# Kernel optimization log

Measured on AMD Instinct MI355X. Metric: run time of the kernel, lower is better.

## Reference

```python
import jax
import jax.numpy as jnp
from jax import lax
import numpy as np

INPUT_DIM = 784
HIDDEN_DIM = 1024
BATCH = 256
N_BINS = 10


def setup_inputs() -> dict:
    key = jax.random.key(0)
    k1, k2, k3, k4, k5 = jax.random.split(key, 5)
    # kaiming-normal-ish init scales (faithful in spirit; exact values irrelevant for math)
    W = jax.random.normal(k1, (HIDDEN_DIM, INPUT_DIM), dtype=jnp.float32) * np.sqrt(2.0 / INPUT_DIM)
    c = jnp.zeros((HIDDEN_DIM, 1), dtype=jnp.float32)
    V = jax.random.normal(k2, (INPUT_DIM, HIDDEN_DIM, N_BINS), dtype=jnp.float32) * np.sqrt(2.0 / N_BINS)
    b = jnp.zeros((INPUT_DIM, N_BINS), dtype=jnp.float32)
    x = jax.random.randint(k3, (BATCH, INPUT_DIM), 0, N_BINS, dtype=jnp.int32)
    return {"x": x, "W": W, "c": c, "V": V, "b": b}


def reference(x, W, c, V, b):
    # x: [B, D] int pixel bins; W: [H, D]; c: [H, 1]; V: [D, H, 10]; b: [D, 10]
    B = x.shape[0]
    xf = x.astype(jnp.float32)  # [B, D]
    a0 = jnp.broadcast_to(c[:, 0][None, :], (B, W.shape[0]))  # [B, H]

    def step(a, inp):
        Vi, bi, Wi, xi = inp  # Vi:[H,10], bi:[10], Wi:[H], xi:[B]
        h = jax.nn.sigmoid(a)                       # [B, H]
        p = jax.nn.softmax(h @ Vi + bi, axis=1)     # [B, 10]
        a = a + xi[:, None] * Wi[None, :]           # rank-1 update, matches x_i @ W[:,i].T
        return a, p

    _, p_seq = lax.scan(step, a0, (V, b, W.T, xf.T))  # p_seq: [D, B, 10]
    p_hat = jnp.transpose(p_seq, (1, 2, 0))            # [B, 10, D] == torch.stack(p_hat, dim=2)
    return p_hat
```

## Files before the change

kernel.cpp:

```cpp
#include <hip/hip_runtime.h>
#include <stdint.h>

#define D_DIM 784
#define H_DIM 1024
#define B_DIM 256
#define NBIN  10
#define G_CH  8
#define T_CH  98
#define BT    16
#define BF    4
#define LOG2E 1.4426950408889634f

typedef _Float16 half8_t  __attribute__((ext_vector_type(8)));
typedef __fp16   fp16x2_t __attribute__((ext_vector_type(2)));
typedef float    float4_t __attribute__((ext_vector_type(4)));

__global__ void k_transpose(const float* __restrict__ W, float* __restrict__ Wt2) {
    __shared__ float t[64][65];
    int j0 = blockIdx.x * 64, h0 = blockIdx.y * 64;
    int tj = threadIdx.x & 63, tr = threadIdx.x >> 6;
    int j = j0 + tj;
    #pragma unroll
    for (int r = 0; r < 16; ++r) {
        int hh = tr * 16 + r;
        t[hh][tj] = (j < D_DIM) ? W[(size_t)(h0 + hh) * D_DIM + j] : 0.0f;
    }
    __syncthreads();
    #pragma unroll
    for (int r = 0; r < 16; ++r) {
        int jj = tr * 16 + r;
        int jo = j0 + jj;
        if (jo < D_DIM) Wt2[(size_t)jo * H_DIM + h0 + tj] = t[tj][jj] * LOG2E;
    }
}

__global__ void k_vbprep(const float* __restrict__ V, _Float16* __restrict__ VB) {
    int i   = blockIdx.x;
    int tid = threadIdx.x;
    __shared__ __align__(16) float vsf[H_DIM * NBIN];
    const float4* src = (const float4*)(V + (size_t)i * H_DIM * NBIN);
    #pragma unroll
    for (int q = 0; q < 10; ++q) {
        float4 v = src[q * 256 + tid];
        *((float4*)&vsf[(q * 256 + tid) * 4]) = v;
    }
    __syncthreads();
    #pragma unroll
    for (int q = 0; q < 8; ++q) {
        int pair = q * 256 + tid;
        int kk = pair >> 6, l = pair & 63;
        int n = l & 15, hb = kk * 32 + ((l >> 4) & 3) * 8;
        union { _Float16 h[8]; uint4 u; } o;
        #pragma unroll
        for (int jj = 0; jj < 8; ++jj)
            o.h[jj] = (_Float16)((n < NBIN) ? vsf[(hb + jj) * NBIN + n] : 0.0f);
        ((uint4*)VB)[(size_t)i * 2048 + pair] = o.u;
    }
}

template<typename CT>
__global__ void k_pscan(const float* __restrict__ Wt2, const int* __restrict__ x,
                        const float* __restrict__ c, CT* __restrict__ PA) {
    int b0 = blockIdx.x * BF;
    int h  = blockIdx.y * 256 + threadIdx.x;
    __shared__ float xs[BF][D_DIM];
    for (int q = threadIdx.x; q < BF * (D_DIM / 4); q += 256) {
        int bb = q / (D_DIM / 4), r = q % (D_DIM / 4);
        int4 xi = ((const int4*)(x + (size_t)(b0 + bb) * D_DIM))[r];
        float4 xf = make_float4((float)xi.x, (float)xi.y, (float)xi.z, (float)xi.w);
        *((float4*)&xs[bb][r * 4]) = xf;
    }
    float acc[BF];
    float cv = c[h] * LOG2E;
    #pragma unroll
    for (int bb = 0; bb < BF; ++bb) acc[bb] = cv;
    __syncthreads();
    for (int t = 0; t < T_CH; ++t) {
        #pragma unroll
        for (int bb = 0; bb < BF; ++bb)
            PA[((size_t)t * B_DIM + b0 + bb) * H_DIM + h] = (CT)acc[bb];
        #pragma unroll
        for (int j = 0; j < G_CH; ++j) {
            float wv = Wt2[(size_t)(t * G_CH + j) * H_DIM + h];
            #pragma unroll
            for (int bb = 0; bb < BF; ++bb)
                acc[bb] += xs[bb][t * G_CH + j] * wv;
        }
    }
}

template<typename CT>
__global__ __launch_bounds__(256, 2)
void k_main(const float* __restrict__ Wt2, const _Float16* __restrict__ VB,
            const CT* __restrict__ PA, const int* __restrict__ x,
            const float* __restrict__ bias, float* __restrict__ out) {
    int bt  = blockIdx.x;
    int tc  = blockIdx.y;
    int tid = threadIdx.x;
    int w   = tid >> 6;
    int l   = tid & 63;
    int bl  = l & 15;
    int kg  = l >> 4;
    int bg  = bt * BT + bl;
    int i0  = tc * G_CH;

    __shared__ __align__(16) float wlds[G_CH][H_DIM];
    __shared__ float red[2][4][64][5];
    __shared__ float bs[G_CH][16];
    __shared__ __align__(16) float plds[BT][NBIN][12];

    {
        int ii = tid >> 4, n = tid & 15;
        if (ii < G_CH) bs[ii][n] = (n < NBIN) ? bias[(size_t)(i0 + ii) * NBIN + n] : 0.0f;
    }
    {
        #pragma unroll
        for (int r = 0; r < G_CH; ++r) {
            float4 v = ((const float4*)(Wt2 + (size_t)(i0 + r) * H_DIM))[tid];
            *((float4*)&wlds[r][tid * 4]) = v;
        }
    }
    float xvf[G_CH];
    {
        const int4* xp = (const int4*)(x + (size_t)bg * D_DIM + i0);
        int4 x0 = xp[0], x1 = xp[1];
        xvf[0] = (float)x0.x; xvf[1] = (float)x0.y; xvf[2] = (float)x0.z; xvf[3] = (float)x0.w;
        xvf[4] = (float)x1.x; xvf[5] = (float)x1.y; xvf[6] = (float)x1.z; xvf[7] = (float)x1.w;
    }
    float a[8][8];
    {
        const CT* src = PA + ((size_t)tc * B_DIM + bg) * H_DIM + w * 256 + kg * 8;
        #pragma unroll
        for (int m = 0; m < 8; ++m)
            #pragma unroll
            for (int j = 0; j < 8; ++j)
                a[m][j] = (float)src[m * 32 + j];
    }
    __syncthreads();

    const uint4* vbbase = (const uint4*)VB;
    #pragma unroll 1
    for (int ii = 0; ii < G_CH; ++ii) {
        int i = i0 + ii;
        int par = ii & 1;

        uint4 vb[8];
        const uint4* vbp = vbbase + ((size_t)i * 32 + w * 8) * 64 + l;
        #pragma unroll
        for (int m = 0; m < 8; ++m) vb[m] = vbp[m * 64];

        if (ii > 0) {
            int ip = ii - 1, pp = par ^ 1;
            float tot = red[pp][0][l][w] + red[pp][1][l][w] + red[pp][2][l][w] + red[pp][3][l][w];
            int n = bl;
            float v = (n < NBIN) ? tot + bs[ip][n] : -3.0e38f;
            float vm = v;
            vm = fmaxf(vm, __shfl_xor(vm, 1));
            vm = fmaxf(vm, __shfl_xor(vm, 2));
            vm = fmaxf(vm, __shfl_xor(vm, 4));
            vm = fmaxf(vm, __shfl_xor(vm, 8));
            float e = __builtin_amdgcn_exp2f((v - vm) * LOG2E);
            float ss = e;
            ss += __shfl_xor(ss, 1); ss += __shfl_xor(ss, 2);
            ss += __shfl_xor(ss, 4); ss += __shfl_xor(ss, 8);
            float p = e * __builtin_amdgcn_rcpf(ss);
            if (n < NBIN) plds[kg * 4 + w][n][ip] = p;
        }

        float xf = xvf[ii];
        float4_t cfrag = {0.f, 0.f, 0.f, 0.f};
        #pragma unroll
        for (int m = 0; m < 8; ++m) {
            union { half8_t h8; uint u32[4]; } af;
            #pragma unroll
            for (int p = 0; p < 4; ++p) {
                float s0 = __builtin_amdgcn_rcpf(1.0f + __builtin_amdgcn_exp2f(-a[m][2 * p]));
                float s1 = __builtin_amdgcn_rcpf(1.0f + __builtin_amdgcn_exp2f(-a[m][2 * p + 1]));
                union { fp16x2_t v; uint u; } cv;
                cv.v = __builtin_amdgcn_cvt_pkrtz(s0, s1);
                af.u32[p] = cv.u;
            }
            union { half8_t h8; uint4 u; } bf;
            bf.u = vb[m];
            cfrag = __builtin_amdgcn_mfma_f32_16x16x32_f16(af.h8, bf.h8, cfrag, 0, 0, 0);

            const float4* wrow = (const float4*)&wlds[ii][w * 256 + kg * 8];
            float4 w0 = wrow[m * 8];
            float4 w1 = wrow[m * 8 + 1];
            a[m][0] += xf * w0.x; a[m][1] += xf * w0.y; a[m][2] += xf * w0.z; a[m][3] += xf * w0.w;
            a[m][4] += xf * w1.x; a[m][5] += xf * w1.y; a[m][6] += xf * w1.z; a[m][7] += xf * w1.w;
        }

        red[par][w][l][0] = cfrag[0]; red[par][w][l][1] = cfrag[1];
        red[par][w][l][2] = cfrag[2]; red[par][w][l][3] = cfrag[3];
        __syncthreads();
    }
    {
        int ip = G_CH - 1, pp = (G_CH - 1) & 1;
        float tot = red[pp][0][l][w] + red[pp][1][l][w] + red[pp][2][l][w] + red[pp][3][l][w];
        int n = bl;
        float v = (n < NBIN) ? tot + bs[ip][n] : -3.0e38f;
        float vm = v;
        vm = fmaxf(vm, __shfl_xor(vm, 1));
        vm = fmaxf(vm, __shfl_xor(vm, 2));
        vm = fmaxf(vm, __shfl_xor(vm, 4));
        vm = fmaxf(vm, __shfl_xor(vm, 8));
        float e = __builtin_amdgcn_exp2f((v - vm) * LOG2E);
        float ss = e;
        ss += __shfl_xor(ss, 1); ss += __shfl_xor(ss, 2);
        ss += __shfl_xor(ss, 4); ss += __shfl_xor(ss, 8);
        float p = e * __builtin_amdgcn_rcpf(ss);
        if (n < NBIN) plds[kg * 4 + w][n][ip] = p;
    }
    __syncthreads();

    if (tid < BT * NBIN) {
        int bb = tid / NBIN, n = tid % NBIN;
        size_t base = ((size_t)(bt * BT + bb) * NBIN + n) * D_DIM + i0;
        #pragma unroll
        for (int q = 0; q < 2; ++q) {
            float4 v = *((float4*)&plds[bb][n][q * 4]);
            *((float4*)(out + base + q * 4)) = v;
        }
    }
}

extern "C" void kernel_launch(void* const* d_in, const int* in_sizes, int n_in,
                              void* d_out, int out_size, void* d_ws, size_t ws_size,
                              hipStream_t stream) {
    const int*   x    = (const int*)d_in[0];
    const float* W    = (const float*)d_in[1];
    const float* c    = (const float*)d_in[2];
    const float* V    = (const float*)d_in[3];
    const float* bias = (const float*)d_in[4];
    float* out = (float*)d_out;

    char* ws = (char*)d_ws;
    size_t off = 0;
    float* Wt2 = (float*)(ws + off);
    off += (size_t)D_DIM * H_DIM * sizeof(float);
    off = (off + 255) & ~(size_t)255;
    _Float16* VB = (_Float16*)(ws + off);
    off += (size_t)D_DIM * 32 * 64 * 8 * sizeof(_Float16);
    off = (off + 255) & ~(size_t)255;
    size_t pa_f32 = (size_t)T_CH * B_DIM * H_DIM * sizeof(float);
    bool f32ck = (off + pa_f32) <= ws_size;

    k_transpose<<<dim3(13, 16), 256, 0, stream>>>(W, Wt2);
    k_vbprep<<<dim3(D_DIM), 256, 0, stream>>>(V, VB);

    if (f32ck) {
        float* PA = (float*)(ws + off);
        k_pscan<float><<<dim3(B_DIM / BF, 4), 256, 0, stream>>>(Wt2, x, c, PA);
        k_main<float><<<dim3(B_DIM / BT, T_CH), 256, 0, stream>>>(Wt2, VB, PA, x, bias, out);
    } else {
        _Float16* PA = (_Float16*)(ws + off);
        k_pscan<_Float16><<<dim3(B_DIM / BF, 4), 256, 0, stream>>>(Wt2, x, c, PA);
        k_main<_Float16><<<dim3(B_DIM / BT, T_CH), 256, 0, stream>>>(Wt2, VB, PA, x, bias, out);
    }
}
```

Measured before the change: 210.6 us.

## Store prefix checkpoints and W tile in fp16, halve pscan batch-per-block

```diff
diff --git a/kernel.cpp b/kernel.cpp
--- a/kernel.cpp
+++ b/kernel.cpp
@@ -8,7 +8,7 @@
 #define G_CH  8
 #define T_CH  98
 #define BT    16
-#define BF    4
+#define BF    2
 #define LOG2E 1.4426950408889634f
 
 typedef _Float16 half8_t  __attribute__((ext_vector_type(8)));
@@ -58,9 +58,8 @@
     }
 }
 
-template<typename CT>
 __global__ void k_pscan(const float* __restrict__ Wt2, const int* __restrict__ x,
-                        const float* __restrict__ c, CT* __restrict__ PA) {
+                        const float* __restrict__ c, _Float16* __restrict__ PA) {
     int b0 = blockIdx.x * BF;
     int h  = blockIdx.y * 256 + threadIdx.x;
     __shared__ float xs[BF][D_DIM];
@@ -70,29 +69,23 @@
         float4 xf = make_float4((float)xi.x, (float)xi.y, (float)xi.z, (float)xi.w);
         *((float4*)&xs[bb][r * 4]) = xf;
     }
-    float acc[BF];
-    float cv = c[h] * LOG2E;
-    #pragma unroll
-    for (int bb = 0; bb < BF; ++bb) acc[bb] = cv;
+    float acc0 = c[h] * LOG2E, acc1 = acc0;
     __syncthreads();
     for (int t = 0; t < T_CH; ++t) {
-        #pragma unroll
-        for (int bb = 0; bb < BF; ++bb)
-            PA[((size_t)t * B_DIM + b0 + bb) * H_DIM + h] = (CT)acc[bb];
+        PA[((size_t)t * B_DIM + b0 + 0) * H_DIM + h] = (_Float16)acc0;
+        PA[((size_t)t * B_DIM + b0 + 1) * H_DIM + h] = (_Float16)acc1;
         #pragma unroll
         for (int j = 0; j < G_CH; ++j) {
             float wv = Wt2[(size_t)(t * G_CH + j) * H_DIM + h];
-            #pragma unroll
-            for (int bb = 0; bb < BF; ++bb)
-                acc[bb] += xs[bb][t * G_CH + j] * wv;
-        }
-    }
-}
-
-template<typename CT>
+            acc0 += xs[0][t * G_CH + j] * wv;
+            acc1 += xs[1][t * G_CH + j] * wv;
+        }
+    }
+}
+
 __global__ __launch_bounds__(256, 2)
 void k_main(const float* __restrict__ Wt2, const _Float16* __restrict__ VB,
-            const CT* __restrict__ PA, const int* __restrict__ x,
+            const _Float16* __restrict__ PA, const int* __restrict__ x,
             const float* __restrict__ bias, float* __restrict__ out) {
     int bt  = blockIdx.x;
     int tc  = blockIdx.y;
@@ -104,7 +97,7 @@
     int bg  = bt * BT + bl;
     int i0  = tc * G_CH;
 
-    __shared__ __align__(16) float wlds[G_CH][H_DIM];
+    __shared__ __align__(16) _Float16 wlds[G_CH][H_DIM];
     __shared__ float red[2][4][64][5];
     __shared__ float bs[G_CH][16];
     __shared__ __align__(16) float plds[BT][NBIN][12];
@@ -117,7 +110,10 @@
         #pragma unroll
         for (int r = 0; r < G_CH; ++r) {
             float4 v = ((const float4*)(Wt2 + (size_t)(i0 + r) * H_DIM))[tid];
-            *((float4*)&wlds[r][tid * 4]) = v;
+            union { fp16x2_t v2[2]; uint2 u; } cv;
+            cv.v2[0] = __builtin_amdgcn_cvt_pkrtz(v.x, v.y);
+            cv.v2[1] = __builtin_amdgcn_cvt_pkrtz(v.z, v.w);
+            *((uint2*)&wlds[r][tid * 4]) = cv.u;
         }
     }
     float xvf[G_CH];
@@ -129,12 +125,13 @@
     }
     float a[8][8];
     {
-        const CT* src = PA + ((size_t)tc * B_DIM + bg) * H_DIM + w * 256 + kg * 8;
-        #pragma unroll
-        for (int m = 0; m < 8; ++m)
+        const _Float16* src = PA + ((size_t)tc * B_DIM + bg) * H_DIM + w * 256 + kg * 8;
+        #pragma unroll
+        for (int m = 0; m < 8; ++m) {
+            half8_t av = *((const half8_t*)(src + m * 32));
             #pragma unroll
-            for (int j = 0; j < 8; ++j)
-                a[m][j] = (float)src[m * 32 + j];
+            for (int j = 0; j < 8; ++j) a[m][j] = (float)av[j];
+        }
     }
     __syncthreads();
 
@@ -184,11 +181,11 @@
             bf.u = vb[m];
             cfrag = __builtin_amdgcn_mfma_f32_16x16x32_f16(af.h8, bf.h8, cfrag, 0, 0, 0);
 
-            const float4* wrow = (const float4*)&wlds[ii][w * 256 + kg * 8];
-            float4 w0 = wrow[m * 8];
-            float4 w1 = wrow[m * 8 + 1];
-            a[m][0] += xf * w0.x; a[m][1] += xf * w0.y; a[m][2] += xf * w0.z; a[m][3] += xf * w0.w;
-            a[m][4] += xf * w1.x; a[m][5] += xf * w1.y; a[m][6] += xf * w1.z; a[m][7] += xf * w1.w;
+            half8_t wh = *((const half8_t*)&wlds[ii][w * 256 + kg * 8 + m * 32]);
+            a[m][0] += xf * (float)wh[0]; a[m][1] += xf * (float)wh[1];
+            a[m][2] += xf * (float)wh[2]; a[m][3] += xf * (float)wh[3];
+            a[m][4] += xf * (float)wh[4]; a[m][5] += xf * (float)wh[5];
+            a[m][6] += xf * (float)wh[6]; a[m][7] += xf * (float)wh[7];
         }
 
         red[par][w][l][0] = cfrag[0]; red[par][w][l][1] = cfrag[1];
@@ -243,19 +240,10 @@
     _Float16* VB = (_Float16*)(ws + off);
     off += (size_t)D_DIM * 32 * 64 * 8 * sizeof(_Float16);
     off = (off + 255) & ~(size_t)255;
-    size_t pa_f32 = (size_t)T_CH * B_DIM * H_DIM * sizeof(float);
-    bool f32ck = (off + pa_f32) <= ws_size;
+    _Float16* PA = (_Float16*)(ws + off);
 
     k_transpose<<<dim3(13, 16), 256, 0, stream>>>(W, Wt2);
     k_vbprep<<<dim3(D_DIM), 256, 0, stream>>>(V, VB);
-
-    if (f32ck) {
-        float* PA = (float*)(ws + off);
-        k_pscan<float><<<dim3(B_DIM / BF, 4), 256, 0, stream>>>(Wt2, x, c, PA);
-        k_main<float><<<dim3(B_DIM / BT, T_CH), 256, 0, stream>>>(Wt2, VB, PA, x, bias, out);
-    } else {
-        _Float16* PA = (_Float16*)(ws + off);
-        k_pscan<_Float16><<<dim3(B_DIM / BF, 4), 256, 0, stream>>>(Wt2, x, c, PA);
-        k_main<_Float16><<<dim3(B_DIM / BT, T_CH), 256, 0, stream>>>(Wt2, VB, PA, x, bias, out);
-    }
-}
+    k_pscan<<<dim3(B_DIM / BF, 4), 256, 0, stream>>>(Wt2, x, c, PA);
+    k_main<<<dim3(B_DIM / BT, T_CH), 256, 0, stream>>>(Wt2, VB, PA, x, bias, out);
+}
```

Result: faster. 202.1 us (-4.0%).
